# Kernel optimization log

Measured on AMD Instinct MI355X. Metric: run time of the kernel, lower is better.

Reference implementation:

```python
import jax, jax.numpy as jnp
import numpy as np

N_NODES = 100000

def prelu(x, alpha):
    return jnp.where(x >= 0, x, alpha * x)

def setup_inputs() -> dict:
    key = jax.random.key(0)
    ks = jax.random.split(key, 8)
    N, E, D = N_NODES, 1600000, 128
    AX = jax.random.normal(ks[0], (N, D), dtype=jnp.float32)
    A_row = jax.random.randint(ks[1], (E,), 0, N, dtype=jnp.int32)
    A_col = jax.random.randint(ks[2], (E,), 0, N, dtype=jnp.int32)
    A_val = jax.random.uniform(ks[3], (E,), dtype=jnp.float32)
    # Xavier-uniform linear weights, zero bias (as in module init)
    lim = float(np.sqrt(6.0 / (D + D)))
    Wr_w = jax.random.uniform(ks[4], (D, D), minval=-lim, maxval=lim, dtype=jnp.float32)
    W_w = jax.random.uniform(ks[5], (D, D), minval=-lim, maxval=lim, dtype=jnp.float32)
    Wr_b = jnp.zeros((D,), dtype=jnp.float32)
    W_b = jnp.zeros((D,), dtype=jnp.float32)
    g_alpha = jnp.full((1,), 0.25, dtype=jnp.float32)    # PReLU default init
    act_alpha = jnp.full((1,), 0.25, dtype=jnp.float32)
    return {"AX": AX, "A_row": A_row, "A_col": A_col, "A_val": A_val,
            "Wr_w": Wr_w, "Wr_b": Wr_b, "W_w": W_w, "W_b": W_b,
            "g_alpha": g_alpha, "act_alpha": act_alpha}

def reference(AX, A_row, A_col, A_val, Wr_w, Wr_b, W_w, W_b, g_alpha, act_alpha):
    # h = g(Wr @ AX)  : [N, H]
    h = prelu(AX @ Wr_w.T + Wr_b, g_alpha)
    # SpMM: temp[i] = sum_{(i,j) in E} A_val * h[j]
    msgs = A_val[:, None] * h[A_col]                       # [E, H] gather
    temp = jax.ops.segment_sum(msgs, A_row, num_segments=N_NODES)
    # act(W @ temp), unsqueeze batch dim
    out = prelu(temp @ W_w.T + W_b, act_alpha)
    return out[None, :, :]
```

## Files before the change

### kernel.cpp

```cpp
#include <hip/hip_runtime.h>
#include <stdint.h>


typedef _Float16 half8 __attribute__((ext_vector_type(8)));
typedef _Float16 half4 __attribute__((ext_vector_type(4)));
typedef float floatx4 __attribute__((ext_vector_type(4)));

#define LDK 136
#define SHIFT 5
#define NBMAX 3200
#define NBLK 256
#define SCT 1024
#define CAP 1024

__global__ __launch_bounds__(256, 2)
void gemm128_prelu(const float* __restrict__ X, const float* __restrict__ W,
                   const float* __restrict__ bias, const float* __restrict__ alpha_p,
                   _Float16* __restrict__ out, int N)
{
    __shared__ _Float16 Xs[128 * LDK];
    __shared__ _Float16 Ws[128 * LDK];
    const int tid = threadIdx.x;
    const int bm  = blockIdx.x * 128;
    const float alpha = *alpha_p;

#pragma unroll
    for (int i = 0; i < 16; ++i) {
        int c   = tid + i * 256;
        int row = c >> 5;
        int coff = (c & 31) * 4;
        float4 f = *(const float4*)(W + row * 128 + coff);
        half4 hv = { (_Float16)f.x, (_Float16)f.y, (_Float16)f.z, (_Float16)f.w };
        *(half4*)(&Ws[row * LDK + coff]) = hv;
    }
#pragma unroll
    for (int i = 0; i < 16; ++i) {
        int c   = tid + i * 256;
        int row = c >> 5;
        int coff = (c & 31) * 4;
        int grow = bm + row;
        half4 hv = {};
        if (grow < N) {
            float4 f = *(const float4*)(X + (size_t)grow * 128 + coff);
            hv[0] = (_Float16)f.x; hv[1] = (_Float16)f.y;
            hv[2] = (_Float16)f.z; hv[3] = (_Float16)f.w;
        }
        *(half4*)(&Xs[row * LDK + coff]) = hv;
    }
    __syncthreads();

    const int wave = tid >> 6;
    const int lane = tid & 63;
    const int l15  = lane & 15;
    const int quad = lane >> 4;

    floatx4 acc[2][8] = {};
#pragma unroll
    for (int k0 = 0; k0 < 128; k0 += 32) {
        half8 a0 = *(const half8*)(&Xs[(wave * 32 +      l15) * LDK + k0 + quad * 8]);
        half8 a1 = *(const half8*)(&Xs[(wave * 32 + 16 + l15) * LDK + k0 + quad * 8]);
        half8 b[8];
#pragma unroll
        for (int n = 0; n < 8; ++n)
            b[n] = *(const half8*)(&Ws[(n * 16 + l15) * LDK + k0 + quad * 8]);
#pragma unroll
        for (int n = 0; n < 8; ++n) {
            acc[0][n] = __builtin_amdgcn_mfma_f32_16x16x32_f16(a0, b[n], acc[0][n], 0, 0, 0);
            acc[1][n] = __builtin_amdgcn_mfma_f32_16x16x32_f16(a1, b[n], acc[1][n], 0, 0, 0);
        }
    }

#pragma unroll
    for (int mt = 0; mt < 2; ++mt) {
#pragma unroll
        for (int n = 0; n < 8; ++n) {
#pragma unroll
            for (int r = 0; r < 4; ++r) {
                int row = bm + wave * 32 + mt * 16 + quad * 4 + r;
                int col = n * 16 + l15;
                if (row < N) {
                    float v = acc[mt][n][r] + bias[col];
                    v = (v >= 0.f) ? v : alpha * v;
                    out[(size_t)row * 128 + col] = (_Float16)v;
                }
            }
        }
    }
}

__global__ __launch_bounds__(SCT)
void bucket_hist(const int* __restrict__ rows, int* __restrict__ hist_g,
                 int E, int chunk, int NB,
                 const float* __restrict__ W, _Float16* __restrict__ W16)
{
    __shared__ int lh[NBMAX];
    int tid = threadIdx.x, blk = blockIdx.x;
    if (blk == 0) {
#pragma unroll
        for (int j = 0; j < 16; ++j) W16[tid + j * 1024] = (_Float16)W[tid + j * 1024];
    }
    for (int i = tid; i < NB; i += SCT) lh[i] = 0;
    __syncthreads();
    int s = blk * chunk, e = min(E, s + chunk);
    for (int i = s + tid; i < e; i += SCT)
        atomicAdd(&lh[rows[i] >> SHIFT], 1);
    __syncthreads();
    for (int b = tid; b < NB; b += SCT)
        hist_g[b * NBLK + blk] = lh[b];
}

__global__ __launch_bounds__(NBLK)
void bucket_scan1(int* __restrict__ hist_g, int* __restrict__ tot)
{
    __shared__ int sd[NBLK];
    int b = blockIdx.x, t = threadIdx.x;
    int v = hist_g[b * NBLK + t];
    sd[t] = v;
    __syncthreads();
    for (int off = 1; off < NBLK; off <<= 1) {
        int x = (t >= off) ? sd[t - off] : 0;
        __syncthreads();
        sd[t] += x;
        __syncthreads();
    }
    hist_g[b * NBLK + t] = sd[t] - v;
    if (t == NBLK - 1) tot[b] = sd[t];
}

__global__ __launch_bounds__(1024)
void bucket_scan2(const int* __restrict__ tot, int* __restrict__ bkt_ptr, int NB, int E)
{
    __shared__ int sd[1024];
    int t = threadIdx.x;
    int v[4]; int s = 0;
#pragma unroll
    for (int j = 0; j < 4; ++j) {
        int idx = t * 4 + j;
        v[j] = (idx < NB) ? tot[idx] : 0;
        s += v[j];
    }
    sd[t] = s;
    __syncthreads();
    for (int off = 1; off < 1024; off <<= 1) {
        int x = (t >= off) ? sd[t - off] : 0;
        __syncthreads();
        sd[t] += x;
        __syncthreads();
    }
    int base = (t == 0) ? 0 : sd[t - 1];
#pragma unroll
    for (int j = 0; j < 4; ++j) {
        int idx = t * 4 + j;
        if (idx < NB) { bkt_ptr[idx] = base; base += v[j]; }
    }
    if (t == 0) bkt_ptr[NB] = E;
}

__global__ __launch_bounds__(SCT)
void bucket_scatter(const int* __restrict__ rows, const int* __restrict__ cols,
                    const float* __restrict__ vals, const int* __restrict__ bkt_ptr,
                    const int* __restrict__ hist_g, uint2* __restrict__ edges,
                    int E, int chunk, int NB)
{
    __shared__ int cur[NBMAX];
    int tid = threadIdx.x, blk = blockIdx.x;
    for (int b = tid; b < NB; b += SCT)
        cur[b] = bkt_ptr[b] + hist_g[b * NBLK + blk];
    __syncthreads();
    int s = blk * chunk, e = min(E, s + chunk);
    for (int i = s + tid; i < e; i += SCT) {
        int r = rows[i];
        int b = r >> SHIFT;
        uint2 ed;
        ed.x = (unsigned)cols[i] | ((unsigned)(r & 31) << 20);
        ed.y = __float_as_uint(vals[i]);
        int p = atomicAdd(&cur[b], 1);
        edges[p] = ed;
    }
}

__global__ __launch_bounds__(256, 6)
void spmm_fused(const int* __restrict__ bkt_ptr, const uint2* __restrict__ edges,
                const _Float16* __restrict__ h, const _Float16* __restrict__ W16,
                const float* __restrict__ bias, const float* __restrict__ alpha_p,
                float* __restrict__ out, int N)
{
    __shared__ uint2 eS[CAP];
    __shared__ _Float16 T[32 * LDK];
    __shared__ int bins[32], startS[33];

    const int tid  = threadIdx.x;
    const int wave = tid >> 6;
    const int lane = tid & 63;
    const int half = lane >> 5;
    const int sl   = lane & 31;
    const int b    = blockIdx.x;
    const int s0   = bkt_ptr[b], e0 = bkt_ptr[b + 1];

    const _Float16* __restrict__ hsl = h + sl * 4;

    float acc[8][4] = {};

    for (int base = s0; base < e0; base += CAP) {
        const int n = min(CAP, e0 - base);
        if (tid < 32) bins[tid] = 0;
        __syncthreads();
        uint2 q[4];
#pragma unroll
        for (int u = 0; u < 4; ++u) {
            int i = tid + u * 256;
            if (i < n) {
                q[u] = edges[base + i];
                atomicAdd(&bins[q[u].x >> 20], 1);
            }
        }
        __syncthreads();
        if (tid < 32) {
            int x = bins[tid];
#pragma unroll
            for (int off = 1; off < 32; off <<= 1) {
                int y = __shfl_up(x, off);
                if (tid >= off) x += y;
            }
            startS[tid + 1] = x;
            if (tid == 0) startS[0] = 0;
            bins[tid] = x - bins[tid];
        }
        __syncthreads();
#pragma unroll
        for (int u = 0; u < 4; ++u) {
            int i = tid + u * 256;
            if (i < n) {
                int p = atomicAdd(&bins[q[u].x >> 20], 1);
                eS[p] = q[u];
            }
        }
        __syncthreads();

#pragma unroll
        for (int j = 0; j < 8; ++j) {
            int r  = wave * 8 + j;
            int rs = startS[r], re = startS[r + 1];
            float a0 = acc[j][0], a1 = acc[j][1], a2 = acc[j][2], a3 = acc[j][3];
            int i = rs;
            for (; i + 7 < re; i += 8) {
                uint2 p0 = eS[i     + half];
                uint2 p1 = eS[i + 2 + half];
                uint2 p2 = eS[i + 4 + half];
                uint2 p3 = eS[i + 6 + half];
                half4 v0 = *(const half4*)(hsl + (size_t)(p0.x & 0xFFFFF) * 128);
                half4 v1 = *(const half4*)(hsl + (size_t)(p1.x & 0xFFFFF) * 128);
                half4 v2 = *(const half4*)(hsl + (size_t)(p2.x & 0xFFFFF) * 128);
                half4 v3 = *(const half4*)(hsl + (size_t)(p3.x & 0xFFFFF) * 128);
                float w0 = __uint_as_float(p0.y), w1 = __uint_as_float(p1.y);
                float w2 = __uint_as_float(p2.y), w3 = __uint_as_float(p3.y);
                a0 += w0 * (float)v0[0]; a1 += w0 * (float)v0[1];
                a2 += w0 * (float)v0[2]; a3 += w0 * (float)v0[3];
                a0 += w1 * (float)v1[0]; a1 += w1 * (float)v1[1];
                a2 += w1 * (float)v1[2]; a3 += w1 * (float)v1[3];
                a0 += w2 * (float)v2[0]; a1 += w2 * (float)v2[1];
                a2 += w2 * (float)v2[2]; a3 += w2 * (float)v2[3];
                a0 += w3 * (float)v3[0]; a1 += w3 * (float)v3[1];
                a2 += w3 * (float)v3[2]; a3 += w3 * (float)v3[3];
            }
            for (; i + 1 < re; i += 2) {
                uint2 p0 = eS[i + half];
                half4 v0 = *(const half4*)(hsl + (size_t)(p0.x & 0xFFFFF) * 128);
                float w0 = __uint_as_float(p0.y);
                a0 += w0 * (float)v0[0]; a1 += w0 * (float)v0[1];
                a2 += w0 * (float)v0[2]; a3 += w0 * (float)v0[3];
            }
            if (i < re) {
                uint2 p0 = eS[i];
                half4 v0 = *(const half4*)(hsl + (size_t)(p0.x & 0xFFFFF) * 128);
                float w0 = half ? 0.f : __uint_as_float(p0.y);
                a0 += w0 * (float)v0[0]; a1 += w0 * (float)v0[1];
                a2 += w0 * (float)v0[2]; a3 += w0 * (float)v0[3];
            }
            acc[j][0] = a0; acc[j][1] = a1; acc[j][2] = a2; acc[j][3] = a3;
        }
        __syncthreads();
    }

#pragma unroll
    for (int j = 0; j < 8; ++j) {
        float m0 = acc[j][0] + __shfl_xor(acc[j][0], 32);
        float m1 = acc[j][1] + __shfl_xor(acc[j][1], 32);
        float m2 = acc[j][2] + __shfl_xor(acc[j][2], 32);
        float m3 = acc[j][3] + __shfl_xor(acc[j][3], 32);
        if (half == 0) {
            half4 o = { (_Float16)m0, (_Float16)m1, (_Float16)m2, (_Float16)m3 };
            *(half4*)(&T[(wave * 8 + j) * LDK + sl * 4]) = o;
        }
    }
    __syncthreads();

    const float alpha = *alpha_p;
    const int l15  = lane & 15;
    const int quad = lane >> 4;
    floatx4 c[2][2] = {};
#pragma unroll
    for (int k0 = 0; k0 < 128; k0 += 32) {
        half8 a0 = *(const half8*)(&T[(     l15) * LDK + k0 + quad * 8]);
        half8 a1 = *(const half8*)(&T[(16 + l15) * LDK + k0 + quad * 8]);
#pragma unroll
        for (int nt = 0; nt < 2; ++nt) {
            int nrow = (wave * 2 + nt) * 16 + l15;
            half8 bf = *(const half8*)(W16 + nrow * 128 + k0 + quad * 8);
            c[0][nt] = __builtin_amdgcn_mfma_f32_16x16x32_f16(a0, bf, c[0][nt], 0, 0, 0);
            c[1][nt] = __builtin_amdgcn_mfma_f32_16x16x32_f16(a1, bf, c[1][nt], 0, 0, 0);
        }
    }
    const int row0 = b << SHIFT;
#pragma unroll
    for (int mt = 0; mt < 2; ++mt) {
#pragma unroll
        for (int nt = 0; nt < 2; ++nt) {
            int col = (wave * 2 + nt) * 16 + l15;
            float bcol = bias[col];
#pragma unroll
            for (int r = 0; r < 4; ++r) {
                int row = row0 + mt * 16 + quad * 4 + r;
                if (row < N) {
                    float v = c[mt][nt][r] + bcol;
                    v = (v >= 0.f) ? v : alpha * v;
                    out[(size_t)row * 128 + col] = v;
                }
            }
        }
    }
}

static inline size_t align256(size_t x) { return (x + 255) & ~(size_t)255; }

extern "C" void kernel_launch(void* const* d_in, const int* in_sizes, int n_in,
                              void* d_out, int out_size, void* d_ws, size_t ws_size,
                              hipStream_t stream)
{
    const float* AX        = (const float*)d_in[0];
    const int*   A_row     = (const int*)  d_in[1];
    const int*   A_col     = (const int*)  d_in[2];
    const float* A_val     = (const float*)d_in[3];
    const float* Wr_w      = (const float*)d_in[4];
    const float* Wr_b      = (const float*)d_in[5];
    const float* W_w       = (const float*)d_in[6];
    const float* W_b       = (const float*)d_in[7];
    const float* g_alpha   = (const float*)d_in[8];
    const float* act_alpha = (const float*)d_in[9];

    const int N = in_sizes[0] / 128;
    const int E = in_sizes[1];
    const int NB = (N + 31) >> SHIFT;
    const int chunk = (E + NBLK - 1) / NBLK;

    char* ws = (char*)d_ws;
    size_t off = 0;
    _Float16* h      = (_Float16*)(ws + off); off += align256((size_t)N * 128 * 2);
    uint2*    edges  = (uint2*)   (ws + off); off += align256((size_t)E * 8);
    int*      hist_g = (int*)     (ws + off); off += align256((size_t)NB * NBLK * 4);
    int*      tot    = (int*)     (ws + off); off += align256((size_t)NB * 4);
    int*      bkt_ptr= (int*)     (ws + off); off += align256((size_t)(NB + 1) * 4);
    _Float16* W16    = (_Float16*)(ws + off); off += align256((size_t)128 * 128 * 2);
    (void)ws_size; (void)n_in; (void)out_size;

    const int gemm_grid = (N + 127) / 128;

    gemm128_prelu<<<gemm_grid, 256, 0, stream>>>(AX, Wr_w, Wr_b, g_alpha, h, N);

    bucket_hist<<<NBLK, SCT, 0, stream>>>(A_row, hist_g, E, chunk, NB, W_w, W16);
    bucket_scan1<<<NB, NBLK, 0, stream>>>(hist_g, tot);
    bucket_scan2<<<1, 1024, 0, stream>>>(tot, bkt_ptr, NB, E);
    bucket_scatter<<<NBLK, SCT, 0, stream>>>(A_row, A_col, A_val, bkt_ptr, hist_g, edges, E, chunk, NB);

    spmm_fused<<<NB, 256, 0, stream>>>(bkt_ptr, edges, h, W16, W_b, act_alpha,
                                       (float*)d_out, N);
}
```

Baseline: 295.3 us.

## Move intra-bucket row sort into separate kernel and use full-wave row gather

Adds a bucket_sort kernel that sorts each bucket's edges by row in place and writes per-row offsets to a new rowofs buffer. spmm_fused drops its LDS sort loop and now has each full wave own one row at a time. Lanes load edge records cooperatively and broadcast them with shuffles, then each lane gathers a half2 slice of h. This removes the LDS edge buffer and syncs from the SpMM kernel, which may help occupancy, at the cost of an extra pass over the edge array and more shuffles. bucket_sort only handles up to CAP edges per bucket, so larger buckets would be silently truncated.

```diff
diff --git a/kernel.cpp b/kernel.cpp
--- a/kernel.cpp
+++ b/kernel.cpp
@@ -4,6 +4,7 @@
 
 typedef _Float16 half8 __attribute__((ext_vector_type(8)));
 typedef _Float16 half4 __attribute__((ext_vector_type(4)));
+typedef _Float16 half2v __attribute__((ext_vector_type(2)));
 typedef float floatx4 __attribute__((ext_vector_type(4)));
 
 #define LDK 136
@@ -179,119 +180,121 @@
     }
 }
 
+__global__ __launch_bounds__(256)
+void bucket_sort(const int* __restrict__ bkt_ptr, uint2* __restrict__ edges,
+                 int* __restrict__ rowofs)
+{
+    __shared__ uint2 eS[CAP];
+    __shared__ int bins[32], startS[33];
+    const int tid = threadIdx.x, b = blockIdx.x;
+    const int s0 = bkt_ptr[b];
+    const int n  = min(bkt_ptr[b + 1] - s0, CAP);
+
+    if (tid < 32) bins[tid] = 0;
+    __syncthreads();
+    uint2 q[4];
+#pragma unroll
+    for (int u = 0; u < 4; ++u) {
+        int i = tid + u * 256;
+        if (i < n) {
+            q[u] = edges[s0 + i];
+            atomicAdd(&bins[q[u].x >> 20], 1);
+        }
+    }
+    __syncthreads();
+    if (tid < 32) {
+        int x = bins[tid];
+#pragma unroll
+        for (int off = 1; off < 32; off <<= 1) {
+            int y = __shfl_up(x, off);
+            if (tid >= off) x += y;
+        }
+        startS[tid + 1] = x;
+        if (tid == 0) startS[0] = 0;
+        bins[tid] = x - bins[tid];
+    }
+    __syncthreads();
+#pragma unroll
+    for (int u = 0; u < 4; ++u) {
+        int i = tid + u * 256;
+        if (i < n) {
+            int p = atomicAdd(&bins[q[u].x >> 20], 1);
+            eS[p] = q[u];
+        }
+    }
+    __syncthreads();
+#pragma unroll
+    for (int u = 0; u < 4; ++u) {
+        int i = tid + u * 256;
+        if (i < n) edges[s0 + i] = eS[i];
+    }
+    if (tid < 33) rowofs[b * 33 + tid] = s0 + startS[tid];
+}
+
 __global__ __launch_bounds__(256, 6)
-void spmm_fused(const int* __restrict__ bkt_ptr, const uint2* __restrict__ edges,
+void spmm_fused(const int* __restrict__ rowofs, const uint2* __restrict__ edges,
                 const _Float16* __restrict__ h, const _Float16* __restrict__ W16,
                 const float* __restrict__ bias, const float* __restrict__ alpha_p,
                 float* __restrict__ out, int N)
 {
-    __shared__ uint2 eS[CAP];
     __shared__ _Float16 T[32 * LDK];
-    __shared__ int bins[32], startS[33];
-
     const int tid  = threadIdx.x;
     const int wave = tid >> 6;
     const int lane = tid & 63;
-    const int half = lane >> 5;
-    const int sl   = lane & 31;
     const int b    = blockIdx.x;
-    const int s0   = bkt_ptr[b], e0 = bkt_ptr[b + 1];
-
-    const _Float16* __restrict__ hsl = h + sl * 4;
-
-    float acc[8][4] = {};
-
-    for (int base = s0; base < e0; base += CAP) {
-        const int n = min(CAP, e0 - base);
-        if (tid < 32) bins[tid] = 0;
-        __syncthreads();
-        uint2 q[4];
-#pragma unroll
-        for (int u = 0; u < 4; ++u) {
-            int i = tid + u * 256;
-            if (i < n) {
-                q[u] = edges[base + i];
-                atomicAdd(&bins[q[u].x >> 20], 1);
+
+    int ro = 0;
+    if (lane < 9) ro = rowofs[b * 33 + wave * 8 + lane];
+    int rs[9];
+#pragma unroll
+    for (int k = 0; k < 9; ++k) rs[k] = __shfl(ro, k);
+
+    const _Float16* __restrict__ hL = h + lane * 2;
+    float acc[8][2] = {};
+
+    for (int wbase = rs[0]; wbase < rs[8]; wbase += 64) {
+        int ii = wbase + lane;
+        uint2 wq = {0u, 0u};
+        if (ii < rs[8]) wq = edges[ii];
+        const int wend = wbase + 64;
+#pragma unroll
+        for (int j = 0; j < 8; ++j) {
+            int lo = rs[j]     > wbase ? rs[j]     : wbase;
+            int hi = rs[j + 1] < wend  ? rs[j + 1] : wend;
+            float a0 = acc[j][0], a1 = acc[j][1];
+            int i = lo;
+            for (; i + 3 < hi; i += 4) {
+                int k0 = i - wbase;
+                unsigned cx0 = __shfl(wq.x, k0),     cy0 = __shfl(wq.y, k0);
+                unsigned cx1 = __shfl(wq.x, k0 + 1), cy1 = __shfl(wq.y, k0 + 1);
+                unsigned cx2 = __shfl(wq.x, k0 + 2), cy2 = __shfl(wq.y, k0 + 2);
+                unsigned cx3 = __shfl(wq.x, k0 + 3), cy3 = __shfl(wq.y, k0 + 3);
+                half2v v0 = *(const half2v*)(hL + (size_t)(cx0 & 0xFFFFF) * 128);
+                half2v v1 = *(const half2v*)(hL + (size_t)(cx1 & 0xFFFFF) * 128);
+                half2v v2 = *(const half2v*)(hL + (size_t)(cx2 & 0xFFFFF) * 128);
+                half2v v3 = *(const half2v*)(hL + (size_t)(cx3 & 0xFFFFF) * 128);
+                float w0 = __uint_as_float(cy0), w1 = __uint_as_float(cy1);
+                float w2 = __uint_as_float(cy2), w3 = __uint_as_float(cy3);
+                a0 += w0 * (float)v0[0]; a1 += w0 * (float)v0[1];
+                a0 += w1 * (float)v1[0]; a1 += w1 * (float)v1[1];
+                a0 += w2 * (float)v2[0]; a1 += w2 * (float)v2[1];
+                a0 += w3 * (float)v3[0]; a1 += w3 * (float)v3[1];
             }
-        }
-        __syncthreads();
-        if (tid < 32) {
-            int x = bins[tid];
-#pragma unroll
-            for (int off = 1; off < 32; off <<= 1) {
-                int y = __shfl_up(x, off);
-                if (tid >= off) x += y;
+            for (; i < hi; ++i) {
+                int k = i - wbase;
+                unsigned cx = __shfl(wq.x, k), cy = __shfl(wq.y, k);
+                half2v v = *(const half2v*)(hL + (size_t)(cx & 0xFFFFF) * 128);
+                float w = __uint_as_float(cy);
+                a0 += w * (float)v[0]; a1 += w * (float)v[1];
             }
-            startS[tid + 1] = x;
-            if (tid == 0) startS[0] = 0;
-            bins[tid] = x - bins[tid];
-        }
-        __syncthreads();
-#pragma unroll
-        for (int u = 0; u < 4; ++u) {
-            int i = tid + u * 256;
-            if (i < n) {
-                int p = atomicAdd(&bins[q[u].x >> 20], 1);
-                eS[p] = q[u];
-            }
-        }
-        __syncthreads();
-
-#pragma unroll
-        for (int j = 0; j < 8; ++j) {
-            int r  = wave * 8 + j;
-            int rs = startS[r], re = startS[r + 1];
-            float a0 = acc[j][0], a1 = acc[j][1], a2 = acc[j][2], a3 = acc[j][3];
-            int i = rs;
-            for (; i + 7 < re; i += 8) {
-                uint2 p0 = eS[i     + half];
-                uint2 p1 = eS[i + 2 + half];
-                uint2 p2 = eS[i + 4 + half];
-                uint2 p3 = eS[i + 6 + half];
-                half4 v0 = *(const half4*)(hsl + (size_t)(p0.x & 0xFFFFF) * 128);
-                half4 v1 = *(const half4*)(hsl + (size_t)(p1.x & 0xFFFFF) * 128);
-                half4 v2 = *(const half4*)(hsl + (size_t)(p2.x & 0xFFFFF) * 128);
-                half4 v3 = *(const half4*)(hsl + (size_t)(p3.x & 0xFFFFF) * 128);
-                float w0 = __uint_as_float(p0.y), w1 = __uint_as_float(p1.y);
-                float w2 = __uint_as_float(p2.y), w3 = __uint_as_float(p3.y);
-                a0 += w0 * (float)v0[0]; a1 += w0 * (float)v0[1];
-                a2 += w0 * (float)v0[2]; a3 += w0 * (float)v0[3];
-                a0 += w1 * (float)v1[0]; a1 += w1 * (float)v1[1];
-                a2 += w1 * (float)v1[2]; a3 += w1 * (float)v1[3];
-                a0 += w2 * (float)v2[0]; a1 += w2 * (float)v2[1];
-                a2 += w2 * (float)v2[2]; a3 += w2 * (float)v2[3];
-                a0 += w3 * (float)v3[0]; a1 += w3 * (float)v3[1];
-                a2 += w3 * (float)v3[2]; a3 += w3 * (float)v3[3];
-            }
-            for (; i + 1 < re; i += 2) {
-                uint2 p0 = eS[i + half];
-                half4 v0 = *(const half4*)(hsl + (size_t)(p0.x & 0xFFFFF) * 128);
-                float w0 = __uint_as_float(p0.y);
-                a0 += w0 * (float)v0[0]; a1 += w0 * (float)v0[1];
-                a2 += w0 * (float)v0[2]; a3 += w0 * (float)v0[3];
-            }
-            if (i < re) {
-                uint2 p0 = eS[i];
-                half4 v0 = *(const half4*)(hsl + (size_t)(p0.x & 0xFFFFF) * 128);
-                float w0 = half ? 0.f : __uint_as_float(p0.y);
-                a0 += w0 * (float)v0[0]; a1 += w0 * (float)v0[1];
-                a2 += w0 * (float)v0[2]; a3 += w0 * (float)v0[3];
-            }
-            acc[j][0] = a0; acc[j][1] = a1; acc[j][2] = a2; acc[j][3] = a3;
-        }
-        __syncthreads();
+            acc[j][0] = a0; acc[j][1] = a1;
+        }
     }
 
 #pragma unroll
     for (int j = 0; j < 8; ++j) {
-        float m0 = acc[j][0] + __shfl_xor(acc[j][0], 32);
-        float m1 = acc[j][1] + __shfl_xor(acc[j][1], 32);
-        float m2 = acc[j][2] + __shfl_xor(acc[j][2], 32);
-        float m3 = acc[j][3] + __shfl_xor(acc[j][3], 32);
-        if (half == 0) {
-            half4 o = { (_Float16)m0, (_Float16)m1, (_Float16)m2, (_Float16)m3 };
-            *(half4*)(&T[(wave * 8 + j) * LDK + sl * 4]) = o;
-        }
+        half2v o = { (_Float16)acc[j][0], (_Float16)acc[j][1] };
+        *(half2v*)(&T[(wave * 8 + j) * LDK + lane * 2]) = o;
     }
     __syncthreads();
 
@@ -360,6 +363,7 @@
     int*      hist_g = (int*)     (ws + off); off += align256((size_t)NB * NBLK * 4);
     int*      tot    = (int*)     (ws + off); off += align256((size_t)NB * 4);
     int*      bkt_ptr= (int*)     (ws + off); off += align256((size_t)(NB + 1) * 4);
+    int*      rowofs = (int*)     (ws + off); off += align256((size_t)NB * 33 * 4);
     _Float16* W16    = (_Float16*)(ws + off); off += align256((size_t)128 * 128 * 2);
     (void)ws_size; (void)n_in; (void)out_size;
 
@@ -371,7 +375,8 @@
     bucket_scan1<<<NB, NBLK, 0, stream>>>(hist_g, tot);
     bucket_scan2<<<1, 1024, 0, stream>>>(tot, bkt_ptr, NB, E);
     bucket_scatter<<<NBLK, SCT, 0, stream>>>(A_row, A_col, A_val, bkt_ptr, hist_g, edges, E, chunk, NB);
-
-    spmm_fused<<<NB, 256, 0, stream>>>(bkt_ptr, edges, h, W16, W_b, act_alpha,
+    bucket_sort<<<NB, 256, 0, stream>>>(bkt_ptr, edges, rowofs);
+
+    spmm_fused<<<NB, 256, 0, stream>>>(rowofs, edges, h, W16, W_b, act_alpha,
                                        (float*)d_out, N);
 }
```

Measured after the change: 294.6 us. Within noise of the previous version (-0.2%).
